# Optimization experiments

Hardware: AMD Instinct MI355X
Metric: run time of the kernel (lower is better)

Reference implementation:

```python
import jax, jax.numpy as jnp
import numpy as np

HEADS = 16
D_HID = 64
N_EMBED = HEADS * D_HID  # 1024; also must equal k_len for the final out @ v


def setup_inputs() -> dict:
    key = jax.random.key(0)
    kq, kk, kv, km = jax.random.split(key, 4)
    B, QL, KL = 4, 2048, 1024
    q = jax.random.normal(kq, (B, QL, N_EMBED), dtype=jnp.float32)
    k = jax.random.normal(kk, (B, KL, N_EMBED), dtype=jnp.float32)
    v = jax.random.normal(kv, (B, KL, N_EMBED), dtype=jnp.float32)
    mask = jax.random.randint(km, (B, QL, 1, KL), 0, 2, dtype=jnp.int32)
    return {"q": q, "k": k, "v": v, "mask": mask}


def reference(q, k, v, mask):
    B, QL, E = q.shape
    KL = k.shape[1]
    H, D = HEADS, D_HID
    qh = q.reshape(B, QL, H, D)
    kh = k.reshape(B, KL, H, D)
    vh = v.reshape(B, KL, H, D)
    # energy: (B, q, h, k), softmax over key axis (dim=3 in the original)
    energy = jnp.einsum('nqhd,nkhd->nqhk', qh, kh)
    energy = jnp.where(mask == 0, jnp.float32(-1e20), energy)
    attention = jax.nn.softmax(energy / jnp.sqrt(jnp.float32(E)), axis=3)
    out = jnp.einsum('nqhk,nkhd->nqhd', attention, vh).reshape(B, QL, H * D)
    # second softmax over the model dim (self.softmax = nn.Softmax(dim=-1))
    out = jax.nn.softmax(out, axis=-1)
    # out @ v : (B, QL, E) @ (B, KL==E, E) -> (B, QL, E)
    v2 = jnp.matmul(out, v)
    return (v2, out)
```

## Files before the change

### kernel.cpp

```cpp
#include <hip/hip_runtime.h>
#include <hip/hip_bf16.h>
#include <stdint.h>

#define HEADS 16
#define DH 64
#define NE 1024
#define BB 4
#define QL 2048
#define KLEN 1024

typedef __attribute__((ext_vector_type(8))) short bf16x8;
typedef __attribute__((ext_vector_type(4))) float f32x4;
typedef unsigned short u16;
typedef unsigned int u32;
typedef unsigned long long u64;

__device__ __forceinline__ u16 f2b(float f){
  union { float f; unsigned u; } v; v.f = f;
  unsigned r = v.u + 0x7fffu + ((v.u >> 16) & 1u);
  return (u16)(r >> 16);
}
__device__ __forceinline__ u32 pack2(float a, float b){
  return (u32)f2b(a) | ((u32)f2b(b) << 16);
}
__device__ __forceinline__ u32 cvtpk(float a, float b){
  u32 r; asm("v_cvt_pk_bf16_f32 %0, %1, %2" : "=v"(r) : "v"(a), "v"(b)); return r;
}
__device__ __forceinline__ void gload16(const void* g, void* l){
  __builtin_amdgcn_global_load_lds((const __attribute__((address_space(1))) u32*)g,
                                   (__attribute__((address_space(3))) u32*)l, 16, 0, 0);
}

__global__ __launch_bounds__(256) void kpack_kernel(const float* __restrict__ k,
    u16* __restrict__ kp){
  int id = blockIdx.x * 256 + threadIdx.x;
  int u = id & 511, kt = (id >> 9) & 15, h = (id >> 13) & 15, b = id >> 17;
  int row = u >> 3, blk = u & 7, d0 = ((blk ^ (row & 7)) << 3);
  const float* src = k + ((size_t)(b * KLEN + kt * 64 + row)) * NE + h * DH + d0;
  float4 f0 = *(const float4*)src;
  float4 f1 = *(const float4*)(src + 4);
  uint4 o;
  o.x = pack2(f0.x, f0.y); o.y = pack2(f0.z, f0.w);
  o.z = pack2(f1.x, f1.y); o.w = pack2(f1.z, f1.w);
  ((uint4*)kp)[id] = o;
}

__global__ __launch_bounds__(256) void vpack_kernel(const float* __restrict__ v,
    u16* __restrict__ vp){
  __shared__ __attribute__((aligned(16))) u16 t[64][72];
  const int b = blockIdx.z, h = blockIdx.y, kt = blockIdx.x;
  const int tid = threadIdx.x;
  {
    int key = tid >> 2, dseg = (tid & 3) * 16;
    const float* src = v + ((size_t)(b * KLEN + kt * 64 + key)) * NE + h * DH + dseg;
#pragma unroll
    for (int i = 0; i < 16; i += 4){
      float4 f = *(const float4*)(src + i);
      t[dseg + i + 0][key] = f2b(f.x); t[dseg + i + 1][key] = f2b(f.y);
      t[dseg + i + 2][key] = f2b(f.z); t[dseg + i + 3][key] = f2b(f.w);
    }
  }
  __syncthreads();
  {
    int row = tid >> 2, p2 = (tid & 3) * 2;
    u16* dst = vp + ((size_t)((b * HEADS + h) * 16 + kt)) * 4096;
#pragma unroll
    for (int e = 0; e < 2; e++){
      int blk = p2 + e, sb = blk ^ (row & 7);
      uint4 d4 = *(const uint4*)&t[row][sb * 8];
      *(uint4*)(dst + (row * 8 + blk) * 8) = d4;
    }
  }
}

__global__ __launch_bounds__(256) void mbits_kernel(const int* __restrict__ mask,
    u64* __restrict__ mb){
  int t = blockIdx.x * 256 + threadIdx.x;
  u64 bal = __ballot(mask[t] != 0);
  if ((threadIdx.x & 63) == 0) mb[t >> 6] = bal;
}

__global__ __launch_bounds__(256) void attn1_kernel(
    const float* __restrict__ q, const u16* __restrict__ kp,
    const u16* __restrict__ vp, const u64* __restrict__ mb,
    float* __restrict__ out1){
  __shared__ __attribute__((aligned(16))) u16 Kt[4096];
  __shared__ __attribute__((aligned(16))) u16 Vt[4096];
  __shared__ __attribute__((aligned(16))) u16 Pt[4][16][72];
  const int b = blockIdx.z, h = blockIdx.y, q0 = blockIdx.x * 64;
  const int tid = threadIdx.x, w = tid >> 6, l = tid & 63;
  const int lq = l & 15, g = l >> 4;
  const int qrow = q0 + w * 16 + lq;
  const float C2 = 0.0450842200278f;

  bf16x8 bq0, bq1;
  {
    const float* qsrc = q + ((size_t)b * QL + qrow) * NE + h * DH + g * 8;
    float4 f0 = *(const float4*)(qsrc);
    float4 f1 = *(const float4*)(qsrc + 4);
    float4 f2 = *(const float4*)(qsrc + 32);
    float4 f3 = *(const float4*)(qsrc + 36);
    bq0[0]=(short)f2b(f0.x*C2); bq0[1]=(short)f2b(f0.y*C2); bq0[2]=(short)f2b(f0.z*C2); bq0[3]=(short)f2b(f0.w*C2);
    bq0[4]=(short)f2b(f1.x*C2); bq0[5]=(short)f2b(f1.y*C2); bq0[6]=(short)f2b(f1.z*C2); bq0[7]=(short)f2b(f1.w*C2);
    bq1[0]=(short)f2b(f2.x*C2); bq1[1]=(short)f2b(f2.y*C2); bq1[2]=(short)f2b(f2.z*C2); bq1[3]=(short)f2b(f2.w*C2);
    bq1[4]=(short)f2b(f3.x*C2); bq1[5]=(short)f2b(f3.y*C2); bq1[6]=(short)f2b(f3.z*C2); bq1[7]=(short)f2b(f3.w*C2);
  }

  const f32x4 fz = {0.f, 0.f, 0.f, 0.f};
  f32x4 accO[4];
#pragma unroll
  for (int t2 = 0; t2 < 4; t2++) accO[t2] = fz;
  float lsum = 0.f;

  const u64* mrow = mb + ((size_t)b * QL + qrow) * (KLEN / 64);
  const u16* kT0 = kp + ((size_t)((b * HEADS + h) * 16)) * 4096;
  const u16* vT0 = vp + ((size_t)((b * HEADS + h) * 16)) * 4096;
  const int blkA = g ^ (lq & 7);
  const int bK0 = lq * 128 + blkA * 16;
  const int bK1 = lq * 128 + (blkA ^ 4) * 16;
  char* KtC = (char*)Kt;
  char* VtC = (char*)Vt;

  for (int kt = 0; kt < 16; ++kt){
    __syncthreads();
    const u16* ks = kT0 + kt * 4096;
    const u16* vs = vT0 + kt * 4096;
    gload16(ks + (size_t)tid * 8,         KtC + w * 1024);
    gload16(ks + (size_t)(256 + tid) * 8, KtC + 4096 + w * 1024);
    gload16(vs + (size_t)tid * 8,         VtC + w * 1024);
    gload16(vs + (size_t)(256 + tid) * 8, VtC + 4096 + w * 1024);
    u64 mw = mrow[kt];
    __syncthreads();

    f32x4 s[4];
#pragma unroll
    for (int c = 0; c < 4; c++) s[c] = fz;
#pragma unroll
    for (int c = 0; c < 4; c++){
      bf16x8 a0 = *(const bf16x8*)(KtC + bK0 + c * 2048);
      bf16x8 a1 = *(const bf16x8*)(KtC + bK1 + c * 2048);
      s[c] = __builtin_amdgcn_mfma_f32_16x16x32_bf16(a0, bq0, s[c], 0, 0, 0);
      s[c] = __builtin_amdgcn_mfma_f32_16x16x32_bf16(a1, bq1, s[c], 0, 0, 0);
    }

    u32 mlo = (u32)(mw >> (4 * g));
    u32 mhi = (u32)(mw >> (4 * g + 32));
    float ps = 0.f;
    u32 pw[8];
#pragma unroll
    for (int c2 = 0; c2 < 2; c2++){
      u32 mm = c2 ? mhi : mlo;
#pragma unroll
      for (int cc = 0; cc < 2; cc++){
        int c = c2 * 2 + cc;
        float p[4];
#pragma unroll
        for (int r = 0; r < 4; r++){
          float sv = ((mm >> (16 * cc + r)) & 1u) ? s[c][r] : -1.0e30f;
          p[r] = __builtin_amdgcn_exp2f(sv);
        }
        ps += (p[0] + p[1]) + (p[2] + p[3]);
        pw[2 * c]     = cvtpk(p[0], p[1]);
        pw[2 * c + 1] = cvtpk(p[2], p[3]);
      }
    }
    lsum += ps;

#pragma unroll
    for (int c = 0; c < 4; c++){
      uint2 u2; u2.x = pw[2 * c]; u2.y = pw[2 * c + 1];
      *(uint2*)&Pt[w][lq][16 * c + 4 * g] = u2;
    }
    bf16x8 ap0 = *(const bf16x8*)&Pt[w][lq][g * 8];
    bf16x8 ap1 = *(const bf16x8*)&Pt[w][lq][32 + g * 8];

#pragma unroll
    for (int t2 = 0; t2 < 4; t2++){
      bf16x8 bv0 = *(const bf16x8*)(VtC + bK0 + t2 * 2048);
      bf16x8 bv1 = *(const bf16x8*)(VtC + bK1 + t2 * 2048);
      accO[t2] = __builtin_amdgcn_mfma_f32_16x16x32_bf16(ap0, bv0, accO[t2], 0, 0, 0);
      accO[t2] = __builtin_amdgcn_mfma_f32_16x16x32_bf16(ap1, bv1, accO[t2], 0, 0, 0);
    }
  }

  lsum += __shfl_xor(lsum, 16, 64);
  lsum += __shfl_xor(lsum, 32, 64);
  float li0 = 1.f / __shfl(lsum, 4 * g + 0, 64);
  float li1 = 1.f / __shfl(lsum, 4 * g + 1, 64);
  float li2 = 1.f / __shfl(lsum, 4 * g + 2, 64);
  float li3 = 1.f / __shfl(lsum, 4 * g + 3, 64);
  float* op = out1 + ((size_t)b * QL + q0 + w * 16) * NE + h * DH;
#pragma unroll
  for (int t2 = 0; t2 < 4; t2++){
    op[(4*g+0) * NE + t2 * 16 + lq] = accO[t2][0] * li0;
    op[(4*g+1) * NE + t2 * 16 + lq] = accO[t2][1] * li1;
    op[(4*g+2) * NE + t2 * 16 + lq] = accO[t2][2] * li2;
    op[(4*g+3) * NE + t2 * 16 + lq] = accO[t2][3] * li3;
  }
}

__global__ __launch_bounds__(256) void softmax2_kernel(float* __restrict__ o){
  const int row = blockIdx.x, tid = threadIdx.x;
  float* p = o + (size_t)row * NE + tid * 4;
  float4 x = *(const float4*)p;
  float mx = fmaxf(fmaxf(x.x, x.y), fmaxf(x.z, x.w));
#pragma unroll
  for (int off = 32; off >= 1; off >>= 1) mx = fmaxf(mx, __shfl_xor(mx, off, 64));
  __shared__ float red[8];
  const int wv = tid >> 6;
  if ((tid & 63) == 0) red[wv] = mx;
  __syncthreads();
  mx = fmaxf(fmaxf(red[0], red[1]), fmaxf(red[2], red[3]));
  float e0 = __expf(x.x - mx), e1 = __expf(x.y - mx);
  float e2 = __expf(x.z - mx), e3 = __expf(x.w - mx);
  float s = (e0 + e1) + (e2 + e3);
#pragma unroll
  for (int off = 32; off >= 1; off >>= 1) s += __shfl_xor(s, off, 64);
  if ((tid & 63) == 0) red[4 + wv] = s;
  __syncthreads();
  s = (red[4] + red[5]) + (red[6] + red[7]);
  float inv = 1.f / s;
  x.x = e0 * inv; x.y = e1 * inv; x.z = e2 * inv; x.w = e3 * inv;
  *(float4*)p = x;
}

__global__ __launch_bounds__(256) void gemm3_kernel(const float* __restrict__ w2,
    const u16* __restrict__ vp, float* __restrict__ v2){
  __shared__ __attribute__((aligned(16))) u16 Wt[4096];
  __shared__ __attribute__((aligned(16))) u16 Vt3[4096];
  const int b = blockIdx.z, q0 = blockIdx.y * 64, n0 = blockIdx.x * 64;
  const int tid = threadIdx.x, w = tid >> 6, l = tid & 63;
  const int lq = l & 15, g = l >> 4;
  const int blkA = g ^ (lq & 7);
  const int bK0 = lq * 128 + blkA * 16;
  const int bK1 = lq * 128 + (blkA ^ 4) * 16;
  char* WtC = (char*)Wt;
  char* VtC = (char*)Vt3;
  const f32x4 fz = {0.f, 0.f, 0.f, 0.f};
  f32x4 acc[4];
#pragma unroll
  for (int t2 = 0; t2 < 4; t2++) acc[t2] = fz;
  const float* wsrc0 = w2 + ((size_t)b * QL + q0) * NE;
  const u16* vT0 = vp + ((size_t)((b * HEADS + (n0 >> 6)) * 16)) * 4096;
  const int rr = tid >> 4, cc = tid & 15;

  for (int ksv = 0; ksv < 16; ++ksv){
    __syncthreads();
#pragma unroll
    for (int pp = 0; pp < 4; pp++){
      int r2 = pp * 16 + rr;
      float4 f = *(const float4*)(wsrc0 + (size_t)r2 * NE + ksv * 64 + cc * 4);
      int blkL = (cc >> 1) ^ (r2 & 7);
      uint2 u2; u2.x = cvtpk(f.x, f.y); u2.y = cvtpk(f.z, f.w);
      *(uint2*)(WtC + (r2 * 8 + blkL) * 16 + (cc & 1) * 8) = u2;
    }
    const u16* vs = vT0 + ksv * 4096;
    gload16(vs + (size_t)tid * 8,         VtC + w * 1024);
    gload16(vs + (size_t)(256 + tid) * 8, VtC + 4096 + w * 1024);
    __syncthreads();
    bf16x8 a0 = *(const bf16x8*)(WtC + w * 2048 + bK0);
    bf16x8 a1 = *(const bf16x8*)(WtC + w * 2048 + bK1);
#pragma unroll
    for (int t2 = 0; t2 < 4; t2++){
      bf16x8 b0 = *(const bf16x8*)(VtC + bK0 + t2 * 2048);
      bf16x8 b1 = *(const bf16x8*)(VtC + bK1 + t2 * 2048);
      acc[t2] = __builtin_amdgcn_mfma_f32_16x16x32_bf16(a0, b0, acc[t2], 0, 0, 0);
      acc[t2] = __builtin_amdgcn_mfma_f32_16x16x32_bf16(a1, b1, acc[t2], 0, 0, 0);
    }
  }
  float* op = v2 + ((size_t)b * QL + q0 + w * 16) * NE + n0;
#pragma unroll
  for (int t2 = 0; t2 < 4; t2++){
#pragma unroll
    for (int r = 0; r < 4; r++){
      op[(4 * g + r) * NE + t2 * 16 + lq] = acc[t2][r];
    }
  }
}

extern "C" void kernel_launch(void* const* d_in, const int* in_sizes, int n_in,
                              void* d_out, int out_size, void* d_ws, size_t ws_size,
                              hipStream_t stream){
  const float* q = (const float*)d_in[0];
  const float* k = (const float*)d_in[1];
  const float* v = (const float*)d_in[2];
  const int* mask = (const int*)d_in[3];
  float* v2 = (float*)d_out;
  float* out2 = v2 + (size_t)BB * QL * NE;

  u16* kp = (u16*)d_ws;
  u16* vpk = kp + (size_t)BB * KLEN * NE;
  u64* mbp = (u64*)(vpk + (size_t)BB * KLEN * NE);

  kpack_kernel<<<2048, 256, 0, stream>>>(k, kp);
  vpack_kernel<<<dim3(16, HEADS, BB), 256, 0, stream>>>(v, vpk);
  mbits_kernel<<<BB * QL * KLEN / 256, 256, 0, stream>>>(mask, mbp);
  attn1_kernel<<<dim3(QL / 64, HEADS, BB), 256, 0, stream>>>(q, kp, vpk, mbp, out2);
  softmax2_kernel<<<BB * QL, 256, 0, stream>>>(out2);
  gemm3_kernel<<<dim3(NE / 64, QL / 64, BB), 256, 0, stream>>>(out2, vpk, v2);
}
```

Measured before the change: 156.2 us.

## Double-buffer attention and GEMM tiles, MFMA row sums, pre-packed bf16 softmax output

The attention kernel now double-buffers K/V tiles in shared memory, so the next tile's loads overlap the current tile's MFMAs and one barrier per iteration is removed. Masking becomes a bitwise AND on the packed bf16 probabilities using a 16-entry LUT, and row sums come from an extra MFMA against a ones vector instead of scalar adds and shuffles. softmax2 also writes a swizzled bf16 copy of its output, which a new double-buffered gemm3f kernel consumes directly, avoiding fp32 loads and conversion in the final GEMM. That path runs only when the workspace is at least 34 MiB, and the row sum is now taken over bf16-rounded probabilities.

```diff
diff --git a/kernel.cpp b/kernel.cpp
--- a/kernel.cpp
+++ b/kernel.cpp
@@ -84,14 +84,22 @@
     const float* __restrict__ q, const u16* __restrict__ kp,
     const u16* __restrict__ vp, const u64* __restrict__ mb,
     float* __restrict__ out1){
-  __shared__ __attribute__((aligned(16))) u16 Kt[4096];
-  __shared__ __attribute__((aligned(16))) u16 Vt[4096];
+  __shared__ __attribute__((aligned(16))) u16 Kt[2][4096];
+  __shared__ __attribute__((aligned(16))) u16 Vt[2][4096];
   __shared__ __attribute__((aligned(16))) u16 Pt[4][16][72];
+  __shared__ u64 LUT[16];
   const int b = blockIdx.z, h = blockIdx.y, q0 = blockIdx.x * 64;
   const int tid = threadIdx.x, w = tid >> 6, l = tid & 63;
   const int lq = l & 15, g = l >> 4;
   const int qrow = q0 + w * 16 + lq;
   const float C2 = 0.0450842200278f;
+
+  if (tid < 16){
+    u32 n = tid;
+    u32 m0 = (n & 1 ? 0xFFFFu : 0u) | (n & 2 ? 0xFFFF0000u : 0u);
+    u32 m1 = (n & 4 ? 0xFFFFu : 0u) | (n & 8 ? 0xFFFF0000u : 0u);
+    LUT[n] = (u64)m0 | ((u64)m1 << 32);
+  }
 
   bf16x8 bq0, bq1;
   {
@@ -110,7 +118,9 @@
   f32x4 accO[4];
 #pragma unroll
   for (int t2 = 0; t2 < 4; t2++) accO[t2] = fz;
-  float lsum = 0.f;
+  f32x4 accL = fz;
+  const short one_bf = (short)0x3F80;
+  const bf16x8 ones = {one_bf, one_bf, one_bf, one_bf, one_bf, one_bf, one_bf, one_bf};
 
   const u64* mrow = mb + ((size_t)b * QL + qrow) * (KLEN / 64);
   const u16* kT0 = kp + ((size_t)((b * HEADS + h) * 16)) * 4096;
@@ -121,50 +131,61 @@
   char* KtC = (char*)Kt;
   char* VtC = (char*)Vt;
 
+  gload16(kT0 + (size_t)tid * 8,         KtC + w * 1024);
+  gload16(kT0 + (size_t)(256 + tid) * 8, KtC + 4096 + w * 1024);
+  gload16(vT0 + (size_t)tid * 8,         VtC + w * 1024);
+  gload16(vT0 + (size_t)(256 + tid) * 8, VtC + 4096 + w * 1024);
+
+  int cur = 0;
   for (int kt = 0; kt < 16; ++kt){
     __syncthreads();
-    const u16* ks = kT0 + kt * 4096;
-    const u16* vs = vT0 + kt * 4096;
-    gload16(ks + (size_t)tid * 8,         KtC + w * 1024);
-    gload16(ks + (size_t)(256 + tid) * 8, KtC + 4096 + w * 1024);
-    gload16(vs + (size_t)tid * 8,         VtC + w * 1024);
-    gload16(vs + (size_t)(256 + tid) * 8, VtC + 4096 + w * 1024);
+    if (kt < 15){
+      const u16* ksn = kT0 + (size_t)(kt + 1) * 4096;
+      const u16* vsn = vT0 + (size_t)(kt + 1) * 4096;
+      char* Kd = KtC + (cur ^ 1) * 8192;
+      char* Vd = VtC + (cur ^ 1) * 8192;
+      gload16(ksn + (size_t)tid * 8,         Kd + w * 1024);
+      gload16(ksn + (size_t)(256 + tid) * 8, Kd + 4096 + w * 1024);
+      gload16(vsn + (size_t)tid * 8,         Vd + w * 1024);
+      gload16(vsn + (size_t)(256 + tid) * 8, Vd + 4096 + w * 1024);
+    }
     u64 mw = mrow[kt];
-    __syncthreads();
+    const char* Kb = KtC + cur * 8192;
+    const char* Vb = VtC + cur * 8192;
 
     f32x4 s[4];
 #pragma unroll
     for (int c = 0; c < 4; c++) s[c] = fz;
 #pragma unroll
     for (int c = 0; c < 4; c++){
-      bf16x8 a0 = *(const bf16x8*)(KtC + bK0 + c * 2048);
-      bf16x8 a1 = *(const bf16x8*)(KtC + bK1 + c * 2048);
+      bf16x8 a0 = *(const bf16x8*)(Kb + bK0 + c * 2048);
+      bf16x8 a1 = *(const bf16x8*)(Kb + bK1 + c * 2048);
       s[c] = __builtin_amdgcn_mfma_f32_16x16x32_bf16(a0, bq0, s[c], 0, 0, 0);
       s[c] = __builtin_amdgcn_mfma_f32_16x16x32_bf16(a1, bq1, s[c], 0, 0, 0);
     }
 
-    u32 mlo = (u32)(mw >> (4 * g));
-    u32 mhi = (u32)(mw >> (4 * g + 32));
-    float ps = 0.f;
     u32 pw[8];
 #pragma unroll
-    for (int c2 = 0; c2 < 2; c2++){
-      u32 mm = c2 ? mhi : mlo;
-#pragma unroll
-      for (int cc = 0; cc < 2; cc++){
-        int c = c2 * 2 + cc;
-        float p[4];
-#pragma unroll
-        for (int r = 0; r < 4; r++){
-          float sv = ((mm >> (16 * cc + r)) & 1u) ? s[c][r] : -1.0e30f;
-          p[r] = __builtin_amdgcn_exp2f(sv);
-        }
-        ps += (p[0] + p[1]) + (p[2] + p[3]);
-        pw[2 * c]     = cvtpk(p[0], p[1]);
-        pw[2 * c + 1] = cvtpk(p[2], p[3]);
-      }
-    }
-    lsum += ps;
+    for (int c = 0; c < 4; c++){
+      float p0 = __builtin_amdgcn_exp2f(s[c][0]);
+      float p1 = __builtin_amdgcn_exp2f(s[c][1]);
+      float p2 = __builtin_amdgcn_exp2f(s[c][2]);
+      float p3 = __builtin_amdgcn_exp2f(s[c][3]);
+      pw[2 * c]     = cvtpk(p0, p1);
+      pw[2 * c + 1] = cvtpk(p2, p3);
+    }
+    {
+      u32 mwlo = (u32)mw, mwhi = (u32)(mw >> 32);
+      int s0 = 4 * g;
+      u64 M0 = LUT[(mwlo >> s0) & 0xFu];
+      u64 M1 = LUT[(mwlo >> (s0 + 16)) & 0xFu];
+      u64 M2 = LUT[(mwhi >> s0) & 0xFu];
+      u64 M3 = LUT[(mwhi >> (s0 + 16)) & 0xFu];
+      pw[0] &= (u32)M0; pw[1] &= (u32)(M0 >> 32);
+      pw[2] &= (u32)M1; pw[3] &= (u32)(M1 >> 32);
+      pw[4] &= (u32)M2; pw[5] &= (u32)(M2 >> 32);
+      pw[6] &= (u32)M3; pw[7] &= (u32)(M3 >> 32);
+    }
 
 #pragma unroll
     for (int c = 0; c < 4; c++){
@@ -174,21 +195,23 @@
     bf16x8 ap0 = *(const bf16x8*)&Pt[w][lq][g * 8];
     bf16x8 ap1 = *(const bf16x8*)&Pt[w][lq][32 + g * 8];
 
+    accL = __builtin_amdgcn_mfma_f32_16x16x32_bf16(ap0, ones, accL, 0, 0, 0);
+    accL = __builtin_amdgcn_mfma_f32_16x16x32_bf16(ap1, ones, accL, 0, 0, 0);
+
 #pragma unroll
     for (int t2 = 0; t2 < 4; t2++){
-      bf16x8 bv0 = *(const bf16x8*)(VtC + bK0 + t2 * 2048);
-      bf16x8 bv1 = *(const bf16x8*)(VtC + bK1 + t2 * 2048);
+      bf16x8 bv0 = *(const bf16x8*)(Vb + bK0 + t2 * 2048);
+      bf16x8 bv1 = *(const bf16x8*)(Vb + bK1 + t2 * 2048);
       accO[t2] = __builtin_amdgcn_mfma_f32_16x16x32_bf16(ap0, bv0, accO[t2], 0, 0, 0);
       accO[t2] = __builtin_amdgcn_mfma_f32_16x16x32_bf16(ap1, bv1, accO[t2], 0, 0, 0);
     }
-  }
-
-  lsum += __shfl_xor(lsum, 16, 64);
-  lsum += __shfl_xor(lsum, 32, 64);
-  float li0 = 1.f / __shfl(lsum, 4 * g + 0, 64);
-  float li1 = 1.f / __shfl(lsum, 4 * g + 1, 64);
-  float li2 = 1.f / __shfl(lsum, 4 * g + 2, 64);
-  float li3 = 1.f / __shfl(lsum, 4 * g + 3, 64);
+    cur ^= 1;
+  }
+
+  float li0 = 1.f / accL[0];
+  float li1 = 1.f / accL[1];
+  float li2 = 1.f / accL[2];
+  float li3 = 1.f / accL[3];
   float* op = out1 + ((size_t)b * QL + q0 + w * 16) * NE + h * DH;
 #pragma unroll
   for (int t2 = 0; t2 < 4; t2++){
@@ -199,7 +222,8 @@
   }
 }
 
-__global__ __launch_bounds__(256) void softmax2_kernel(float* __restrict__ o){
+__global__ __launch_bounds__(256) void softmax2_kernel(float* __restrict__ o,
+    u16* __restrict__ wp){
   const int row = blockIdx.x, tid = threadIdx.x;
   float* p = o + (size_t)row * NE + tid * 4;
   float4 x = *(const float4*)p;
@@ -222,6 +246,75 @@
   float inv = 1.f / s;
   x.x = e0 * inv; x.y = e1 * inv; x.z = e2 * inv; x.w = e3 * inv;
   *(float4*)p = x;
+  if (wp){
+    int b = row >> 11, qi = row & 2047;
+    int qt = qi >> 6, rw = qi & 63;
+    int ktile = tid >> 4, db = (tid >> 1) & 7, half = tid & 1;
+    size_t tile = (size_t)((b * 32 + qt) * 16 + ktile);
+    char* dst = (char*)wp + tile * 8192 + rw * 128 + ((db ^ (rw & 7)) * 16) + half * 8;
+    uint2 u2; u2.x = cvtpk(x.x, x.y); u2.y = cvtpk(x.z, x.w);
+    *(uint2*)dst = u2;
+  }
+}
+
+__global__ __launch_bounds__(256) void gemm3f_kernel(const u16* __restrict__ wp,
+    const u16* __restrict__ vp, float* __restrict__ v2){
+  __shared__ __attribute__((aligned(16))) u16 Wt[2][4096];
+  __shared__ __attribute__((aligned(16))) u16 Vt3[2][4096];
+  const int b = blockIdx.z, qt = blockIdx.y, h3 = blockIdx.x;
+  const int tid = threadIdx.x, w = tid >> 6, l = tid & 63;
+  const int lq = l & 15, g = l >> 4;
+  const int blkA = g ^ (lq & 7);
+  const int bK0 = lq * 128 + blkA * 16;
+  const int bK1 = lq * 128 + (blkA ^ 4) * 16;
+  char* WtC = (char*)Wt;
+  char* VtC = (char*)Vt3;
+  const f32x4 fz = {0.f, 0.f, 0.f, 0.f};
+  f32x4 acc[4];
+#pragma unroll
+  for (int t2 = 0; t2 < 4; t2++) acc[t2] = fz;
+  const u16* wT0 = wp + ((size_t)((b * 32 + qt) * 16)) * 4096;
+  const u16* vT0 = vp + ((size_t)((b * HEADS + h3) * 16)) * 4096;
+
+  gload16(wT0 + (size_t)tid * 8,         WtC + w * 1024);
+  gload16(wT0 + (size_t)(256 + tid) * 8, WtC + 4096 + w * 1024);
+  gload16(vT0 + (size_t)tid * 8,         VtC + w * 1024);
+  gload16(vT0 + (size_t)(256 + tid) * 8, VtC + 4096 + w * 1024);
+
+  int cur = 0;
+  for (int ksv = 0; ksv < 16; ++ksv){
+    __syncthreads();
+    if (ksv < 15){
+      const u16* wsn = wT0 + (size_t)(ksv + 1) * 4096;
+      const u16* vsn = vT0 + (size_t)(ksv + 1) * 4096;
+      char* Wd = WtC + (cur ^ 1) * 8192;
+      char* Vd = VtC + (cur ^ 1) * 8192;
+      gload16(wsn + (size_t)tid * 8,         Wd + w * 1024);
+      gload16(wsn + (size_t)(256 + tid) * 8, Wd + 4096 + w * 1024);
+      gload16(vsn + (size_t)tid * 8,         Vd + w * 1024);
+      gload16(vsn + (size_t)(256 + tid) * 8, Vd + 4096 + w * 1024);
+    }
+    const char* Wb = WtC + cur * 8192;
+    const char* Vb = VtC + cur * 8192;
+    bf16x8 a0 = *(const bf16x8*)(Wb + w * 2048 + bK0);
+    bf16x8 a1 = *(const bf16x8*)(Wb + w * 2048 + bK1);
+#pragma unroll
+    for (int t2 = 0; t2 < 4; t2++){
+      bf16x8 b0 = *(const bf16x8*)(Vb + bK0 + t2 * 2048);
+      bf16x8 b1 = *(const bf16x8*)(Vb + bK1 + t2 * 2048);
+      acc[t2] = __builtin_amdgcn_mfma_f32_16x16x32_bf16(a0, b0, acc[t2], 0, 0, 0);
+      acc[t2] = __builtin_amdgcn_mfma_f32_16x16x32_bf16(a1, b1, acc[t2], 0, 0, 0);
+    }
+    cur ^= 1;
+  }
+  float* op = v2 + ((size_t)b * QL + qt * 64 + w * 16) * NE + h3 * 64;
+#pragma unroll
+  for (int t2 = 0; t2 < 4; t2++){
+#pragma unroll
+    for (int r = 0; r < 4; r++){
+      op[(4 * g + r) * NE + t2 * 16 + lq] = acc[t2][r];
+    }
+  }
 }
 
 __global__ __launch_bounds__(256) void gemm3_kernel(const float* __restrict__ w2,
@@ -288,14 +381,21 @@
   float* v2 = (float*)d_out;
   float* out2 = v2 + (size_t)BB * QL * NE;
 
-  u16* kp = (u16*)d_ws;
-  u16* vpk = kp + (size_t)BB * KLEN * NE;
-  u64* mbp = (u64*)(vpk + (size_t)BB * KLEN * NE);
+  char* wsb = (char*)d_ws;
+  u16* kp  = (u16*)wsb;
+  u16* vpk = (u16*)(wsb + (8u << 20));
+  u64* mbp = (u64*)(wsb + (16u << 20));
+  u16* wpk = (u16*)(wsb + (17u << 20));
+  const bool fast = ws_size >= (34ull << 20);
 
   kpack_kernel<<<2048, 256, 0, stream>>>(k, kp);
   vpack_kernel<<<dim3(16, HEADS, BB), 256, 0, stream>>>(v, vpk);
   mbits_kernel<<<BB * QL * KLEN / 256, 256, 0, stream>>>(mask, mbp);
   attn1_kernel<<<dim3(QL / 64, HEADS, BB), 256, 0, stream>>>(q, kp, vpk, mbp, out2);
-  softmax2_kernel<<<BB * QL, 256, 0, stream>>>(out2);
-  gemm3_kernel<<<dim3(NE / 64, QL / 64, BB), 256, 0, stream>>>(out2, vpk, v2);
-}
+  softmax2_kernel<<<BB * QL, 256, 0, stream>>>(out2, fast ? wpk : (u16*)nullptr);
+  if (fast){
+    gemm3f_kernel<<<dim3(NE / 64, QL / 64, BB), 256, 0, stream>>>(wpk, vpk, v2);
+  } else {
+    gemm3_kernel<<<dim3(NE / 64, QL / 64, BB), 256, 0, stream>>>(out2, vpk, v2);
+  }
+}
```

Result: faster. 144.6 us (-7.4%).
